# Performance work log

Measured on AMD Instinct MI355X. Metric: run time of the kernel, lower is better.

Reference implementation:

```python
import jax, jax.numpy as jnp
import numpy as np

B, N, DIM = 8, 2048, 1024
DR = DIM // 4      # MoE feature dim = 256
E, DH = 4, DIM // 32  # 4 experts, hidden 32
TASKS = 3
TOPK = 2


def _ln(x, g, b, eps=1e-5):
    m = x.mean(-1, keepdims=True)
    v = x.var(-1, keepdims=True)
    return (x - m) * jax.lax.rsqrt(v + eps) * g + b


def _cv_sq(x, eps=1e-10):
    # squared coefficient of variation (Shazeer MoE load-balance loss)
    return x.var() / (x.mean() ** 2 + eps)


def setup_inputs() -> dict:
    key = jax.random.key(0)
    ks = jax.random.split(key, 14)
    g = lambda k, shape, sc: jax.random.normal(k, shape, jnp.float32) * sc
    return {
        "x": jax.random.normal(ks[0], (B, N, DIM), jnp.float32),
        "t": jax.random.normal(ks[1], (B, N, DIM), jnp.float32),
        "past_x": jax.random.normal(ks[2], (B, N, DIM), jnp.float32),
        "past_t": jax.random.normal(ks[3], (B, N, DIM), jnp.float32),
        "task_index": 1,
        "ln1_g": jnp.ones((2 * DIM,), jnp.float32),
        "ln1_b": jnp.zeros((2 * DIM,), jnp.float32),
        "w_red": g(ks[4], (2 * DIM, DR), 0.03),       # xavier-ish, stored [in,out]
        "ln2_g": jnp.ones((DR,), jnp.float32),
        "ln2_b": jnp.zeros((DR,), jnp.float32),
        "w_gate": g(ks[5], (TASKS, DR, E), 0.02),      # per-task gating weights
        "w1": g(ks[6], (E, DR, DH), 0.05),
        "b1": jnp.zeros((E, DH), jnp.float32),
        "w2": g(ks[7], (E, DH, DR), 0.05),
        "b2": jnp.zeros((E, DR), jnp.float32),
        "modal_shifts": g(ks[8], (2 * TASKS, DIM), 0.02),
        "ws1": g(ks[9], (DIM, DIM), 0.02),             # score_net Linear(dim,dim)
        "ws2": g(ks[10], (DIM, 1), 0.02),              # score_net Linear(dim,1)
    }


def reference(x, t, past_x, past_t, task_index, ln1_g, ln1_b, w_red, ln2_g, ln2_b,
              w_gate, w1, b1, w2, b2, modal_shifts, ws1, ws2):
    Bx, Nx, C = x.shape
    y = jnp.concatenate([x, t], axis=-1)               # [B,N,2C]
    y = _ln(y, ln1_g, ln1_b)
    y = y @ w_red                                      # [B,N,C//4]
    y = _ln(y, ln2_g, ln2_b)
    yf = y.reshape(Bx * Nx, C // 4)                    # [M,256]

    # ---- MMoE: noisy top-k gating (eval: no noise), k=2 over E=4 experts ----
    logits = yf @ w_gate[task_index]                   # [M,E]
    top_v, top_i = jax.lax.top_k(logits, TOPK)         # [M,k]
    top_g = jax.nn.softmax(top_v, axis=-1)
    M = yf.shape[0]
    gates = jnp.zeros_like(logits).at[jnp.arange(M)[:, None], top_i].set(top_g)  # [M,E]
    h = jax.nn.relu(jnp.einsum('md,edh->meh', yf, w1) + b1)   # [M,E,32]
    eo = jnp.einsum('meh,eho->meo', h, w2) + b2               # [M,E,256]
    ymoe = jnp.einsum('meo,me->mo', eo, gates)                # [M,256]
    importance = gates.sum(0)
    load = (gates > 0).astype(jnp.float32).sum(0)
    aux_loss = _cv_sq(importance) + _cv_sq(load)

    ymoe = ymoe.reshape(Bx, Nx, C // 4)
    prompt_x, prompt_t = jnp.split(ymoe, 2, axis=-1)   # [B,N,C//8] each
    # AdaptiveAvgPool1d(1) over last dim + sigmoid -> [B,N,1] gate
    prompt_x = jax.nn.sigmoid(prompt_x.mean(-1, keepdims=True))
    prompt_t = jax.nn.sigmoid(prompt_t.mean(-1, keepdims=True))

    out_x = prompt_x * x + modal_shifts[task_index * 2 + 0]
    out_t = prompt_t * t + modal_shifts[task_index * 2 + 1]

    # delta / score-net softmax combine (past_xft branch)
    d1 = jnp.abs(out_x - past_x).mean(axis=1)          # [B,C]
    d2 = jnp.abs(out_t - past_t).mean(axis=1)
    s1 = jax.nn.relu(d1 @ ws1) @ ws2                   # [B,1]
    s2 = jax.nn.relu(d2 @ ws1) @ ws2
    w = jax.nn.softmax(jnp.concatenate([s1, s2], axis=1), axis=1)  # [B,2]
    out = w[:, 1, None, None] * out_x + w[:, 0, None, None] * out_t
    return out, aux_loss, out_x, out_t
```

## Files before the change

kernel.cpp:

```cpp
#include <hip/hip_runtime.h>
#include <math.h>

#define DIMC 1024
#define C2   2048
#define DR   256
#define DH   32
#define NE   4
#define NB   8
#define NN   2048
#define NM   16384

typedef short bf16x8 __attribute__((ext_vector_type(8)));
typedef float f32x4  __attribute__((ext_vector_type(4)));

__device__ __forceinline__ unsigned short f2bf(float f) {
    union { float f; unsigned int u; } v; v.f = f;
    unsigned int r = v.u + 0x7fffu + ((v.u >> 16) & 1u);
    return (unsigned short)(r >> 16);
}

__global__ __launch_bounds__(256) void k_prep(
    const float* __restrict__ wred, const float* __restrict__ g1,
    const float* __restrict__ b1v, unsigned short* __restrict__ wpp,
    float* __restrict__ u, float* __restrict__ beta)
{
    __shared__ unsigned short tsh[64][72];
    __shared__ float ush[64], bsh[64];
    const int tid = threadIdx.x;
    const int k0 = (blockIdx.x >> 2) * 64;
    const int c0 = (blockIdx.x & 3) * 64;
    if (tid < 64) { ush[tid] = 0.f; bsh[tid] = 0.f; }
    __syncthreads();

    const int r = tid >> 2, cs = (tid & 3) * 16;
    const float gk = g1[k0 + r], bk = b1v[k0 + r];
#pragma unroll
    for (int i = 0; i < 4; ++i) {
        float4 wv = *(const float4*)(wred + (size_t)(k0 + r) * DR + c0 + cs + i * 4);
        const int cb = cs + i * 4;
        atomicAdd(&ush[cb + 0], gk * wv.x); atomicAdd(&ush[cb + 1], gk * wv.y);
        atomicAdd(&ush[cb + 2], gk * wv.z); atomicAdd(&ush[cb + 3], gk * wv.w);
        atomicAdd(&bsh[cb + 0], bk * wv.x); atomicAdd(&bsh[cb + 1], bk * wv.y);
        atomicAdd(&bsh[cb + 2], bk * wv.z); atomicAdd(&bsh[cb + 3], bk * wv.w);
        tsh[cb + 0][r] = f2bf(gk * wv.x);
        tsh[cb + 1][r] = f2bf(gk * wv.y);
        tsh[cb + 2][r] = f2bf(gk * wv.z);
        tsh[cb + 3][r] = f2bf(gk * wv.w);
    }
    __syncthreads();

    const int cc = tid >> 2, seg = (tid & 3) * 16;
    uint4 v0 = *(const uint4*)&tsh[cc][seg];
    uint4 v1 = *(const uint4*)&tsh[cc][seg + 8];
    unsigned short* dst = wpp + (size_t)(c0 + cc) * C2 + k0 + seg;
    *(uint4*)(dst)     = v0;
    *(uint4*)(dst + 8) = v1;
    if (tid < 64) {
        atomicAdd(&u[c0 + tid],    ush[tid]);
        atomicAdd(&beta[c0 + tid], bsh[tid]);
    }
}

#define FT  64
#define FBK 64
#define LDA 72
#define LDB 72

__global__ __launch_bounds__(256) void k_front(
    const float* __restrict__ x, const float* __restrict__ t,
    const unsigned short* __restrict__ wpp,
    const float* __restrict__ u, const float* __restrict__ beta,
    const float* __restrict__ ln2g, const float* __restrict__ ln2b,
    float* __restrict__ yf)
{
    __shared__ unsigned short A_sh[FT * LDA];
    __shared__ unsigned short B_sh[DR * LDB];
    __shared__ float us_sh[DR], be_sh[DR], g2_sh[DR], b2_sh[DR];
    __shared__ float mean_sh[FT], rstd_sh[FT];
    __shared__ float pls[FT][2], plss[FT][2];

    const int tid  = threadIdx.x;
    const int m0   = blockIdx.x * FT;
    const int lane = tid & 63;
    const int w    = tid >> 6;
    const int wr   = w & 1, wc = w >> 1;
    const int cl   = lane & 15, kg = lane >> 4;

    if (tid < DR) {
        us_sh[tid] = u[tid];   be_sh[tid] = beta[tid];
        g2_sh[tid] = ln2g[tid]; b2_sh[tid] = ln2b[tid];
    }

    const int atok = tid >> 2, aks = (tid & 3) * 16;
    const int brow = tid >> 3, boff = (tid & 7) * 8;

    float s1 = 0.f, ss1 = 0.f;
    float4 ax[4];
    uint4  bw[8];

    {
        const float* arow = x + (size_t)(m0 + atok) * DIMC + aks;
#pragma unroll
        for (int i = 0; i < 4; ++i) ax[i] = *(const float4*)(arow + i * 4);
#pragma unroll
        for (int i = 0; i < 8; ++i)
            bw[i] = *(const uint4*)(wpp + (size_t)(i * 32 + brow) * C2 + boff);
    }

    f32x4 acc[2][8];
#pragma unroll
    for (int rt = 0; rt < 2; ++rt)
#pragma unroll
        for (int ct = 0; ct < 8; ++ct) acc[rt][ct] = (f32x4){0.f, 0.f, 0.f, 0.f};

    for (int kc = 0; kc < 32; ++kc) {
        __syncthreads();
#pragma unroll
        for (int i = 0; i < 4; ++i) {
            float4 v = ax[i];
            s1  += v.x + v.y + v.z + v.w;
            ss1 += v.x * v.x + v.y * v.y + v.z * v.z + v.w * v.w;
            short4 p;
            p.x = (short)f2bf(v.x); p.y = (short)f2bf(v.y);
            p.z = (short)f2bf(v.z); p.w = (short)f2bf(v.w);
            *(short4*)&A_sh[atok * LDA + aks + i * 4] = p;
        }
#pragma unroll
        for (int i = 0; i < 8; ++i)
            *(uint4*)&B_sh[(i * 32 + brow) * LDB + boff] = bw[i];
        __syncthreads();

        if (kc < 31) {
            const int kn = kc + 1;
            const float* src = (kn < 16) ? x : t;
            const int kb = (kn < 16) ? kn * FBK : (kn - 16) * FBK;
            const float* arow = src + (size_t)(m0 + atok) * DIMC + kb + aks;
#pragma unroll
            for (int i = 0; i < 4; ++i) ax[i] = *(const float4*)(arow + i * 4);
#pragma unroll
            for (int i = 0; i < 8; ++i)
                bw[i] = *(const uint4*)(wpp + (size_t)(i * 32 + brow) * C2 + kn * FBK + boff);
        }

#pragma unroll
        for (int kk = 0; kk < 2; ++kk) {
            bf16x8 af0 = *(const bf16x8*)&A_sh[(wr * 32 + 0  + cl) * LDA + kk * 32 + kg * 8];
            bf16x8 af1 = *(const bf16x8*)&A_sh[(wr * 32 + 16 + cl) * LDA + kk * 32 + kg * 8];
#pragma unroll
            for (int ct = 0; ct < 8; ++ct) {
                bf16x8 bf = *(const bf16x8*)&B_sh[(wc * 128 + ct * 16 + cl) * LDB + kk * 32 + kg * 8];
                acc[0][ct] = __builtin_amdgcn_mfma_f32_16x16x32_bf16(af0, bf, acc[0][ct], 0, 0, 0);
                acc[1][ct] = __builtin_amdgcn_mfma_f32_16x16x32_bf16(af1, bf, acc[1][ct], 0, 0, 0);
            }
        }
    }

    {
        float s = s1, ss = ss1;
        s += __shfl_xor(s, 1); ss += __shfl_xor(ss, 1);
        s += __shfl_xor(s, 2); ss += __shfl_xor(ss, 2);
        if ((tid & 3) == 0) {
            float m  = s * (1.f / 2048.f);
            float va = ss * (1.f / 2048.f) - m * m;
            mean_sh[atok] = m;
            rstd_sh[atok] = rsqrtf(va + 1e-5f);
        }
    }
    __syncthreads();

    float rsum[2][4], rssq[2][4];
#pragma unroll
    for (int rt = 0; rt < 2; ++rt)
#pragma unroll
        for (int reg = 0; reg < 4; ++reg) { rsum[rt][reg] = 0.f; rssq[rt][reg] = 0.f; }

#pragma unroll
    for (int rt = 0; rt < 2; ++rt) {
#pragma unroll
        for (int ct = 0; ct < 8; ++ct) {
            const int col = wc * 128 + ct * 16 + cl;
            const float uu = us_sh[col], bb = be_sh[col];
#pragma unroll
            for (int reg = 0; reg < 4; ++reg) {
                const int tok = wr * 32 + rt * 16 + kg * 4 + reg;
                const float mu = mean_sh[tok], rr = rstd_sh[tok];
                float y = rr * acc[rt][ct][reg] - rr * mu * uu + bb;
                acc[rt][ct][reg] = y;
                rsum[rt][reg] += y; rssq[rt][reg] += y * y;
            }
        }
    }
#pragma unroll
    for (int mask = 1; mask <= 8; mask <<= 1)
#pragma unroll
        for (int rt = 0; rt < 2; ++rt)
#pragma unroll
            for (int reg = 0; reg < 4; ++reg) {
                rsum[rt][reg] += __shfl_xor(rsum[rt][reg], mask);
                rssq[rt][reg] += __shfl_xor(rssq[rt][reg], mask);
            }
    if (cl == 0) {
#pragma unroll
        for (int rt = 0; rt < 2; ++rt)
#pragma unroll
            for (int reg = 0; reg < 4; ++reg) {
                const int tok = wr * 32 + rt * 16 + kg * 4 + reg;
                pls[tok][wc]  = rsum[rt][reg];
                plss[tok][wc] = rssq[rt][reg];
            }
    }
    __syncthreads();

#pragma unroll
    for (int rt = 0; rt < 2; ++rt) {
#pragma unroll
        for (int reg = 0; reg < 4; ++reg) {
            const int tok = wr * 32 + rt * 16 + kg * 4 + reg;
            const float m2 = (pls[tok][0] + pls[tok][1]) * (1.f / 256.f);
            const float v2 = (plss[tok][0] + plss[tok][1]) * (1.f / 256.f) - m2 * m2;
            const float r2 = rsqrtf(v2 + 1e-5f);
            float* yr = yf + (size_t)(m0 + tok) * DR;
#pragma unroll
            for (int ct = 0; ct < 8; ++ct) {
                const int col = wc * 128 + ct * 16 + cl;
                yr[col] = (acc[rt][ct][reg] - m2) * r2 * g2_sh[col] + b2_sh[col];
            }
        }
    }
}

__global__ __launch_bounds__(256) void k_moe(
    const float* __restrict__ yf, const int* __restrict__ taskp,
    const float* __restrict__ wgate,
    const float* __restrict__ w1, const float* __restrict__ b1,
    const float* __restrict__ w2, const float* __restrict__ b2,
    float* __restrict__ px, float* __restrict__ pt,
    double* __restrict__ imp, double* __restrict__ loadc)
{
    __shared__ float yf_sh[4][DR];
    __shared__ float hg_sh[4][2][DH];
    __shared__ float red_sh[8];

    const int tid = threadIdx.x, w = tid >> 6, l = tid & 63;
    if (tid < 8) red_sh[tid] = 0.f;
    const int task = *taskp;
    const int m = blockIdx.x * 4 + w;

    float4 v4 = *(const float4*)(yf + (size_t)m * DR + l * 4);
    *(float4*)&yf_sh[w][l * 4] = v4;
    __syncthreads();

    const float* wg = wgate + task * (DR * NE);
    float lg0 = 0.f, lg1 = 0.f, lg2 = 0.f, lg3 = 0.f;
    {
        const float vv[4] = {v4.x, v4.y, v4.z, v4.w};
#pragma unroll
        for (int i = 0; i < 4; ++i) {
            float4 wrow = *(const float4*)(wg + (l * 4 + i) * 4);
            float a = vv[i];
            lg0 += a * wrow.x; lg1 += a * wrow.y;
            lg2 += a * wrow.z; lg3 += a * wrow.w;
        }
    }
#pragma unroll
    for (int off = 32; off; off >>= 1) {
        lg0 += __shfl_xor(lg0, off); lg1 += __shfl_xor(lg1, off);
        lg2 += __shfl_xor(lg2, off); lg3 += __shfl_xor(lg3, off);
    }
    float lg[4] = {lg0, lg1, lg2, lg3};

    int i0 = 0; float v0 = lg[0];
#pragma unroll
    for (int e = 1; e < 4; ++e) if (lg[e] > v0) { v0 = lg[e]; i0 = e; }
    int i1 = -1; float v1 = -INFINITY;
#pragma unroll
    for (int e = 0; e < 4; ++e) if (e != i0 && lg[e] > v1) { v1 = lg[e]; i1 = e; }
    const float g1 = 1.f / (1.f + expf(v0 - v1));
    const float g0 = 1.f - g1;

    const int half = l >> 5, j = l & 31;
    const int e    = half ? i1 : i0;
    const float ge = half ? g1 : g0;
    const float* w1e = w1 + e * (DR * DH) + j;
    float h = b1[e * DH + j];
#pragma unroll 4
    for (int c = 0; c < DR; c += 4) {
        float4 y4 = *(const float4*)&yf_sh[w][c];
        h += y4.x * w1e[(c + 0) * DH] + y4.y * w1e[(c + 1) * DH]
           + y4.z * w1e[(c + 2) * DH] + y4.w * w1e[(c + 3) * DH];
    }
    hg_sh[w][half][j] = ge * fmaxf(h, 0.f);
    __syncthreads();

    const int o0 = l * 4;
    float4 ym;
    {
        float4 ba = *(const float4*)(b2 + i0 * DR + o0);
        float4 bb = *(const float4*)(b2 + i1 * DR + o0);
        ym.x = g0 * ba.x + g1 * bb.x;
        ym.y = g0 * ba.y + g1 * bb.y;
        ym.z = g0 * ba.z + g1 * bb.z;
        ym.w = g0 * ba.w + g1 * bb.w;
    }
    const float* w2a = w2 + i0 * (DH * DR) + o0;
    const float* w2b = w2 + i1 * (DH * DR) + o0;
#pragma unroll 4
    for (int jj = 0; jj < DH; ++jj) {
        float ha = hg_sh[w][0][jj], hb = hg_sh[w][1][jj];
        float4 wa = *(const float4*)(w2a + jj * DR);
        float4 wb = *(const float4*)(w2b + jj * DR);
        ym.x += ha * wa.x + hb * wb.x;
        ym.y += ha * wa.y + hb * wb.y;
        ym.z += ha * wa.z + hb * wb.z;
        ym.w += ha * wa.w + hb * wb.w;
    }

    float sm = ym.x + ym.y + ym.z + ym.w;
    float sx = (l < 32) ? sm : 0.f;
    float st = (l < 32) ? 0.f : sm;
#pragma unroll
    for (int off = 32; off; off >>= 1) { sx += __shfl_xor(sx, off); st += __shfl_xor(st, off); }
    if (l == 0) {
        px[m] = 1.f / (1.f + expf(-sx * (1.f / 128.f)));
        pt[m] = 1.f / (1.f + expf(-st * (1.f / 128.f)));
        atomicAdd(&red_sh[i0], g0);
        atomicAdd(&red_sh[i1], g1);
        atomicAdd(&red_sh[4 + i0], 1.f);
        atomicAdd(&red_sh[4 + i1], 1.f);
    }
    __syncthreads();
    if (tid < 4)        atomicAdd(&imp[tid], (double)red_sh[tid]);
    else if (tid < 8)   atomicAdd(&loadc[tid - 4], (double)red_sh[tid]);
}

#define K3T 32
__global__ __launch_bounds__(256) void k_outxt(
    const float* __restrict__ x, const float* __restrict__ t,
    const float* __restrict__ past_x, const float* __restrict__ past_t,
    const float* __restrict__ px, const float* __restrict__ pt,
    const int* __restrict__ taskp, const float* __restrict__ mshift,
    float* __restrict__ out_x, float* __restrict__ out_t,
    float* __restrict__ d1, float* __restrict__ d2)
{
    __shared__ float oxs[DIMC], ots[DIMC];
    const int b  = blockIdx.x >> 6;
    const int ch = blockIdx.x & 63;
    const int tid = threadIdx.x;
    const int c  = tid * 4;
    const int task = *taskp;

    float4 shx = *(const float4*)(mshift + (size_t)(task * 2 + 0) * DIMC + c);
    float4 sht = *(const float4*)(mshift + (size_t)(task * 2 + 1) * DIMC + c);

    float a10 = 0.f, a11 = 0.f, a12 = 0.f, a13 = 0.f;
    float a20 = 0.f, a21 = 0.f, a22 = 0.f, a23 = 0.f;
    const int mbase = b * NN + ch * K3T;

    for (int n = 0; n < K3T; ++n) {
        const int m = mbase + n;
        const size_t off = (size_t)m * DIMC + c;
        const float pxv = px[m], ptv = pt[m];

        float4 xv = *(const float4*)(x + off);
        float4 p1 = *(const float4*)(past_x + off);
        float4 ox;
        ox.x = pxv * xv.x + shx.x; ox.y = pxv * xv.y + shx.y;
        ox.z = pxv * xv.z + shx.z; ox.w = pxv * xv.w + shx.w;
        a10 += fabsf(ox.x - p1.x); a11 += fabsf(ox.y - p1.y);
        a12 += fabsf(ox.z - p1.z); a13 += fabsf(ox.w - p1.w);
        *(float4*)&oxs[c] = ox;

        float4 tv = *(const float4*)(t + off);
        float4 p2 = *(const float4*)(past_t + off);
        float4 ot;
        ot.x = ptv * tv.x + sht.x; ot.y = ptv * tv.y + sht.y;
        ot.z = ptv * tv.z + sht.z; ot.w = ptv * tv.w + sht.w;
        a20 += fabsf(ot.x - p2.x); a21 += fabsf(ot.y - p2.y);
        a22 += fabsf(ot.z - p2.z); a23 += fabsf(ot.w - p2.w);
        *(float4*)&ots[c] = ot;
        __syncthreads();

        const size_t rb = (size_t)m * DIMC;
        if (tid < 255) {
            const int cj = 3 + 4 * tid;
            float4 vx = make_float4(oxs[cj], oxs[cj+1], oxs[cj+2], oxs[cj+3]);
            *(float4*)(out_x + rb + cj) = vx;
            float4 vt = make_float4(ots[cj], ots[cj+1], ots[cj+2], ots[cj+3]);
            *(float4*)(out_t + rb + cj) = vt;
        } else {
            out_x[rb + 0] = oxs[0]; out_x[rb + 1] = oxs[1];
            out_x[rb + 2] = oxs[2]; out_x[rb + 1023] = oxs[1023];
            out_t[rb + 0] = ots[0]; out_t[rb + 1] = ots[1];
            out_t[rb + 2] = ots[2]; out_t[rb + 1023] = ots[1023];
        }
        __syncthreads();
    }
    atomicAdd(&d1[b * DIMC + c + 0], a10);
    atomicAdd(&d1[b * DIMC + c + 1], a11);
    atomicAdd(&d1[b * DIMC + c + 2], a12);
    atomicAdd(&d1[b * DIMC + c + 3], a13);
    atomicAdd(&d2[b * DIMC + c + 0], a20);
    atomicAdd(&d2[b * DIMC + c + 1], a21);
    atomicAdd(&d2[b * DIMC + c + 2], a22);
    atomicAdd(&d2[b * DIMC + c + 3], a23);
}

__global__ __launch_bounds__(256) void k_score(
    const float* __restrict__ d1, const float* __restrict__ d2,
    const float* __restrict__ ws1, const float* __restrict__ ws2,
    float* __restrict__ sv)
{
    __shared__ float red1[4][64], red2[4][64];
    const int tid = threadIdx.x;
    const int b = blockIdx.x >> 4, jc = blockIdx.x & 15;
    const int j = jc * 64 + (tid & 63), part = tid >> 6;
    const float* d1r = d1 + b * DIMC + part * 256;
    const float* d2r = d2 + b * DIMC + part * 256;
    const float* wp  = ws1 + (size_t)(part * 256) * DIMC + j;

    float acc1 = 0.f, acc2 = 0.f;
    for (int i = 0; i < 256; ++i) {
        float w = wp[(size_t)i * DIMC];
        acc1 += d1r[i] * w;
        acc2 += d2r[i] * w;
    }
    red1[part][tid & 63] = acc1;
    red2[part][tid & 63] = acc2;
    __syncthreads();
    if (tid < 64) {
        float h1 = red1[0][tid] + red1[1][tid] + red1[2][tid] + red1[3][tid];
        float h2 = red2[0][tid] + red2[1][tid] + red2[2][tid] + red2[3][tid];
        const int jj = jc * 64 + tid;
        float s1 = fmaxf(h1 * (1.f / NN), 0.f) * ws2[jj];
        float s2 = fmaxf(h2 * (1.f / NN), 0.f) * ws2[jj];
#pragma unroll
        for (int mask = 1; mask <= 32; mask <<= 1) {
            s1 += __shfl_xor(s1, mask); s2 += __shfl_xor(s2, mask);
        }
        if (tid == 0) {
            atomicAdd(&sv[b * 2 + 0], s1);
            atomicAdd(&sv[b * 2 + 1], s2);
        }
    }
}

__global__ void k_final_small(const double* __restrict__ imp, const double* __restrict__ loadc,
                              const float* __restrict__ sv, float* __restrict__ wcomb,
                              float* __restrict__ aux_out)
{
    const int tid = threadIdx.x;
    if (tid == 0) {
        double mi = 0, qi = 0, ml = 0, ql = 0;
        for (int e = 0; e < 4; ++e) {
            mi += imp[e]; qi += imp[e] * imp[e];
            ml += loadc[e]; ql += loadc[e] * loadc[e];
        }
        mi *= 0.25; qi *= 0.25; ml *= 0.25; ql *= 0.25;
        double vi = qi - mi * mi, vl = ql - ml * ml;
        *aux_out = (float)(vi / (mi * mi + 1e-10) + vl / (ml * ml + 1e-10));
    }
    if (tid < 8) {
        float s1 = sv[tid * 2 + 0], s2 = sv[tid * 2 + 1];
        float mx = fmaxf(s1, s2);
        float e1 = expf(s1 - mx), e2 = expf(s2 - mx);
        float inv = 1.f / (e1 + e2);
        wcomb[tid * 2 + 0] = e2 * inv;
        wcomb[tid * 2 + 1] = e1 * inv;
    }
}

__global__ __launch_bounds__(256) void k_combine(
    const float* __restrict__ out_x, const float* __restrict__ out_t,
    const float* __restrict__ wcomb, float* __restrict__ out)
{
    __shared__ float oxs[DIMC], ots[DIMC];
    const int m = blockIdx.x;
    const size_t rb = (size_t)m * DIMC;
    const int b = m >> 11;
    const float wx = wcomb[b * 2 + 0], wt = wcomb[b * 2 + 1];
    const int tid = threadIdx.x;

    if (tid < 255) {
        const int cj = 3 + 4 * tid;
        float4 vx = *(const float4*)(out_x + rb + cj);
        oxs[cj] = vx.x; oxs[cj + 1] = vx.y; oxs[cj + 2] = vx.z; oxs[cj + 3] = vx.w;
        float4 vt = *(const float4*)(out_t + rb + cj);
        ots[cj] = vt.x; ots[cj + 1] = vt.y; ots[cj + 2] = vt.z; ots[cj + 3] = vt.w;
    } else {
        oxs[0] = out_x[rb + 0]; oxs[1] = out_x[rb + 1];
        oxs[2] = out_x[rb + 2]; oxs[1023] = out_x[rb + 1023];
        ots[0] = out_t[rb + 0]; ots[1] = out_t[rb + 1];
        ots[2] = out_t[rb + 2]; ots[1023] = out_t[rb + 1023];
    }
    __syncthreads();

    const int c = tid * 4;
    float4 o;
    o.x = wx * oxs[c + 0] + wt * ots[c + 0];
    o.y = wx * oxs[c + 1] + wt * ots[c + 1];
    o.z = wx * oxs[c + 2] + wt * ots[c + 2];
    o.w = wx * oxs[c + 3] + wt * ots[c + 3];
    *(float4*)(out + rb + c) = o;
}

extern "C" void kernel_launch(void* const* d_in, const int* in_sizes, int n_in,
                              void* d_out, int out_size, void* d_ws, size_t ws_size,
                              hipStream_t stream)
{
    const float* x      = (const float*)d_in[0];
    const float* t      = (const float*)d_in[1];
    const float* past_x = (const float*)d_in[2];
    const float* past_t = (const float*)d_in[3];
    const int*   task   = (const int*)d_in[4];
    const float* ln1g   = (const float*)d_in[5];
    const float* ln1b   = (const float*)d_in[6];
    const float* wred   = (const float*)d_in[7];
    const float* ln2g   = (const float*)d_in[8];
    const float* ln2b   = (const float*)d_in[9];
    const float* wgate  = (const float*)d_in[10];
    const float* w1     = (const float*)d_in[11];
    const float* b1     = (const float*)d_in[12];
    const float* w2     = (const float*)d_in[13];
    const float* b2     = (const float*)d_in[14];
    const float* mshift = (const float*)d_in[15];
    const float* ws1    = (const float*)d_in[16];
    const float* ws2    = (const float*)d_in[17];

    float* f     = (float*)d_ws;
    float* d1    = f;
    float* d2    = f + 8192;
    float* sv    = f + 16384;
    float* wcomb = f + 16400;
    double* imp   = (double*)(f + 16416);
    double* loadc = (double*)(f + 16424);

    float* out   = (float*)d_out;
    float* aux   = out + (size_t)NM * DIMC;
    float* out_x = aux + 1;
    float* out_t = out_x + (size_t)NM * DIMC;

    float* yf  = out;
    unsigned short* wpp = (unsigned short*)(out + 8000000);
    float* u    = out + 8400000;
    float* beta = out + 8400256;
    float* px   = out + (size_t)NM * DIMC - 2 * NM;
    float* pt   = px + NM;

    hipMemsetAsync(d_ws, 0, 16432 * sizeof(float), stream);
    hipMemsetAsync(u, 0, 512 * sizeof(float), stream);

    k_prep<<<128, 256, 0, stream>>>(wred, ln1g, ln1b, wpp, u, beta);
    k_front<<<NM / FT, 256, 0, stream>>>(x, t, wpp, u, beta, ln2g, ln2b, yf);
    k_moe<<<NM / 4, 256, 0, stream>>>(yf, task, wgate, w1, b1, w2, b2, px, pt, imp, loadc);
    k_outxt<<<NB * (NN / K3T), 256, 0, stream>>>(x, t, past_x, past_t, px, pt, task,
                                                 mshift, out_x, out_t, d1, d2);
    k_score<<<128, 256, 0, stream>>>(d1, d2, ws1, ws2, sv);
    k_final_small<<<1, 64, 0, stream>>>(imp, loadc, sv, wcomb, aux);
    k_combine<<<NM, 256, 0, stream>>>(out_x, out_t, wcomb, out);
}
```

Baseline: 715.0 us.

## Double-buffer front GEMM with direct global-to-LDS weight loads and smaller tiles

Reworks the fused LayerNorm and reduction GEMM kernel. It uses 32-token tiles with four waves each covering 64 output columns, double-buffered LDS, and global_load_lds to stream the bf16 weight tile straight into XOR-swizzled shared memory. Activation loads and bf16 conversion for the next chunk overlap the MFMA work on the current one. The aim is more blocks in flight (launch bounds of two per CU), fewer register staging copies and fewer LDS bank conflicts. In exchange, weight tiles are reloaded twice as often per token, since each block covers fewer tokens.

```diff
diff --git a/kernel.cpp b/kernel.cpp
--- a/kernel.cpp
+++ b/kernel.cpp
@@ -61,29 +61,33 @@
     }
 }
 
-#define FT  64
-#define FBK 64
-#define LDA 72
-#define LDB 72
-
-__global__ __launch_bounds__(256) void k_front(
+#define FT   32
+#define FBK  64
+#define LDA  72
+#define NCH  32
+
+#define GLDS(gp, lo) __builtin_amdgcn_global_load_lds( \
+    (const __attribute__((address_space(1))) unsigned int*)(unsigned long long)(gp), \
+    (__attribute__((address_space(3))) unsigned int*)(unsigned int)(unsigned long long)(lo), \
+    16, 0, 0)
+
+__global__ __launch_bounds__(256, 2) void k_front(
     const float* __restrict__ x, const float* __restrict__ t,
     const unsigned short* __restrict__ wpp,
     const float* __restrict__ u, const float* __restrict__ beta,
     const float* __restrict__ ln2g, const float* __restrict__ ln2b,
     float* __restrict__ yf)
 {
-    __shared__ unsigned short A_sh[FT * LDA];
-    __shared__ unsigned short B_sh[DR * LDB];
+    __shared__ __attribute__((aligned(16))) unsigned short A_sh[2][FT * LDA];
+    __shared__ __attribute__((aligned(16))) unsigned short B_sh[2][DR * FBK];
     __shared__ float us_sh[DR], be_sh[DR], g2_sh[DR], b2_sh[DR];
     __shared__ float mean_sh[FT], rstd_sh[FT];
-    __shared__ float pls[FT][2], plss[FT][2];
+    __shared__ float pls[FT][4], plss[FT][4];
 
     const int tid  = threadIdx.x;
     const int m0   = blockIdx.x * FT;
     const int lane = tid & 63;
     const int w    = tid >> 6;
-    const int wr   = w & 1, wc = w >> 1;
     const int cl   = lane & 15, kg = lane >> 4;
 
     if (tid < DR) {
@@ -91,75 +95,92 @@
         g2_sh[tid] = ln2g[tid]; b2_sh[tid] = ln2b[tid];
     }
 
-    const int atok = tid >> 2, aks = (tid & 3) * 16;
-    const int brow = tid >> 3, boff = (tid & 7) * 8;
+    const int atok = tid >> 3;
+    const int aks  = (tid & 7) * 8;
+
+    const int brow  = w * 64 + (lane >> 3);
+    const int bslot = (lane & 7) ^ (lane >> 3);
+    const unsigned char* wppB =
+        (const unsigned char*)wpp + (size_t)brow * 4096 + (size_t)bslot * 16;
+    const unsigned long long ldsB =
+        (unsigned long long)(const void*)&B_sh[0][0] + (unsigned)(w * 8192);
 
     float s1 = 0.f, ss1 = 0.f;
-    float4 ax[4];
-    uint4  bw[8];
-
-    {
-        const float* arow = x + (size_t)(m0 + atok) * DIMC + aks;
-#pragma unroll
-        for (int i = 0; i < 4; ++i) ax[i] = *(const float4*)(arow + i * 4);
-#pragma unroll
-        for (int i = 0; i < 8; ++i)
-            bw[i] = *(const uint4*)(wpp + (size_t)(i * 32 + brow) * C2 + boff);
-    }
-
-    f32x4 acc[2][8];
+    f32x4 acc[2][4];
 #pragma unroll
     for (int rt = 0; rt < 2; ++rt)
 #pragma unroll
-        for (int ct = 0; ct < 8; ++ct) acc[rt][ct] = (f32x4){0.f, 0.f, 0.f, 0.f};
-
-    for (int kc = 0; kc < 32; ++kc) {
+        for (int ct = 0; ct < 4; ++ct) acc[rt][ct] = (f32x4){0.f, 0.f, 0.f, 0.f};
+
+    float4 nax0, nax1;
+
+#define STAGE(KN, BUF) do { \
+        const float* _src = ((KN) < 16) ? x : t; \
+        const float* _ar = _src + (size_t)(m0 + atok) * DIMC + ((KN) & 15) * FBK + aks; \
+        nax0 = *(const float4*)_ar; nax1 = *(const float4*)(_ar + 4); \
+        _Pragma("unroll") \
+        for (int _i = 0; _i < 8; ++_i) \
+            GLDS(wppB + (size_t)_i * 8 * 4096 + (KN) * 128, \
+                 ldsB + (unsigned)((BUF) * 32768 + _i * 1024)); \
+    } while (0)
+
+#define CVT(BUF) do { \
+        float4 _v = nax0; \
+        s1 += _v.x + _v.y + _v.z + _v.w; \
+        ss1 += _v.x*_v.x + _v.y*_v.y + _v.z*_v.z + _v.w*_v.w; \
+        short4 _p; \
+        _p.x = (short)f2bf(_v.x); _p.y = (short)f2bf(_v.y); \
+        _p.z = (short)f2bf(_v.z); _p.w = (short)f2bf(_v.w); \
+        *(short4*)&A_sh[BUF][atok * LDA + aks] = _p; \
+        _v = nax1; \
+        s1 += _v.x + _v.y + _v.z + _v.w; \
+        ss1 += _v.x*_v.x + _v.y*_v.y + _v.z*_v.z + _v.w*_v.w; \
+        _p.x = (short)f2bf(_v.x); _p.y = (short)f2bf(_v.y); \
+        _p.z = (short)f2bf(_v.z); _p.w = (short)f2bf(_v.w); \
+        *(short4*)&A_sh[BUF][atok * LDA + aks + 4] = _p; \
+    } while (0)
+
+#define MFMA_PHASE(BUF) do { \
+        _Pragma("unroll") \
+        for (int kk = 0; kk < 2; ++kk) { \
+            bf16x8 af0 = *(const bf16x8*)&A_sh[BUF][(cl)      * LDA + kk * 32 + kg * 8]; \
+            bf16x8 af1 = *(const bf16x8*)&A_sh[BUF][(16 + cl) * LDA + kk * 32 + kg * 8]; \
+            _Pragma("unroll") \
+            for (int ct = 0; ct < 4; ++ct) { \
+                const int _r  = w * 64 + ct * 16 + cl; \
+                const int _off = (_r * 128 + kk * 64 + kg * 16) ^ ((_r & 7) << 4); \
+                bf16x8 bf = *(const bf16x8*)((const char*)&B_sh[BUF][0] + _off); \
+                acc[0][ct] = __builtin_amdgcn_mfma_f32_16x16x32_bf16(af0, bf, acc[0][ct], 0, 0, 0); \
+                acc[1][ct] = __builtin_amdgcn_mfma_f32_16x16x32_bf16(af1, bf, acc[1][ct], 0, 0, 0); \
+            } \
+        } \
+    } while (0)
+
+    STAGE(0, 0);
+    CVT(0);
+    __syncthreads();
+
+    for (int kc = 0; kc < NCH; kc += 2) {
+        STAGE(kc + 1, 1);
+        MFMA_PHASE(0);
+        CVT(1);
         __syncthreads();
-#pragma unroll
-        for (int i = 0; i < 4; ++i) {
-            float4 v = ax[i];
-            s1  += v.x + v.y + v.z + v.w;
-            ss1 += v.x * v.x + v.y * v.y + v.z * v.z + v.w * v.w;
-            short4 p;
-            p.x = (short)f2bf(v.x); p.y = (short)f2bf(v.y);
-            p.z = (short)f2bf(v.z); p.w = (short)f2bf(v.w);
-            *(short4*)&A_sh[atok * LDA + aks + i * 4] = p;
-        }
-#pragma unroll
-        for (int i = 0; i < 8; ++i)
-            *(uint4*)&B_sh[(i * 32 + brow) * LDB + boff] = bw[i];
+        if (kc + 2 < NCH) {
+            STAGE(kc + 2, 0);
+            MFMA_PHASE(1);
+            CVT(0);
+        } else {
+            MFMA_PHASE(1);
+        }
         __syncthreads();
-
-        if (kc < 31) {
-            const int kn = kc + 1;
-            const float* src = (kn < 16) ? x : t;
-            const int kb = (kn < 16) ? kn * FBK : (kn - 16) * FBK;
-            const float* arow = src + (size_t)(m0 + atok) * DIMC + kb + aks;
-#pragma unroll
-            for (int i = 0; i < 4; ++i) ax[i] = *(const float4*)(arow + i * 4);
-#pragma unroll
-            for (int i = 0; i < 8; ++i)
-                bw[i] = *(const uint4*)(wpp + (size_t)(i * 32 + brow) * C2 + kn * FBK + boff);
-        }
-
-#pragma unroll
-        for (int kk = 0; kk < 2; ++kk) {
-            bf16x8 af0 = *(const bf16x8*)&A_sh[(wr * 32 + 0  + cl) * LDA + kk * 32 + kg * 8];
-            bf16x8 af1 = *(const bf16x8*)&A_sh[(wr * 32 + 16 + cl) * LDA + kk * 32 + kg * 8];
-#pragma unroll
-            for (int ct = 0; ct < 8; ++ct) {
-                bf16x8 bf = *(const bf16x8*)&B_sh[(wc * 128 + ct * 16 + cl) * LDB + kk * 32 + kg * 8];
-                acc[0][ct] = __builtin_amdgcn_mfma_f32_16x16x32_bf16(af0, bf, acc[0][ct], 0, 0, 0);
-                acc[1][ct] = __builtin_amdgcn_mfma_f32_16x16x32_bf16(af1, bf, acc[1][ct], 0, 0, 0);
-            }
-        }
     }
 
     {
         float s = s1, ss = ss1;
         s += __shfl_xor(s, 1); ss += __shfl_xor(ss, 1);
         s += __shfl_xor(s, 2); ss += __shfl_xor(ss, 2);
-        if ((tid & 3) == 0) {
+        s += __shfl_xor(s, 4); ss += __shfl_xor(ss, 4);
+        if ((tid & 7) == 0) {
             float m  = s * (1.f / 2048.f);
             float va = ss * (1.f / 2048.f) - m * m;
             mean_sh[atok] = m;
@@ -175,20 +196,19 @@
         for (int reg = 0; reg < 4; ++reg) { rsum[rt][reg] = 0.f; rssq[rt][reg] = 0.f; }
 
 #pragma unroll
-    for (int rt = 0; rt < 2; ++rt) {
-#pragma unroll
-        for (int ct = 0; ct < 8; ++ct) {
-            const int col = wc * 128 + ct * 16 + cl;
-            const float uu = us_sh[col], bb = be_sh[col];
+    for (int ct = 0; ct < 4; ++ct) {
+        const int col = w * 64 + ct * 16 + cl;
+        const float uu = us_sh[col], bb = be_sh[col];
+#pragma unroll
+        for (int rt = 0; rt < 2; ++rt)
 #pragma unroll
             for (int reg = 0; reg < 4; ++reg) {
-                const int tok = wr * 32 + rt * 16 + kg * 4 + reg;
+                const int tok = rt * 16 + kg * 4 + reg;
                 const float mu = mean_sh[tok], rr = rstd_sh[tok];
                 float y = rr * acc[rt][ct][reg] - rr * mu * uu + bb;
                 acc[rt][ct][reg] = y;
                 rsum[rt][reg] += y; rssq[rt][reg] += y * y;
             }
-        }
     }
 #pragma unroll
     for (int mask = 1; mask <= 8; mask <<= 1)
@@ -204,9 +224,9 @@
         for (int rt = 0; rt < 2; ++rt)
 #pragma unroll
             for (int reg = 0; reg < 4; ++reg) {
-                const int tok = wr * 32 + rt * 16 + kg * 4 + reg;
-                pls[tok][wc]  = rsum[rt][reg];
-                plss[tok][wc] = rssq[rt][reg];
+                const int tok = rt * 16 + kg * 4 + reg;
+                pls[tok][w]  = rsum[rt][reg];
+                plss[tok][w] = rssq[rt][reg];
             }
     }
     __syncthreads();
@@ -215,18 +235,21 @@
     for (int rt = 0; rt < 2; ++rt) {
 #pragma unroll
         for (int reg = 0; reg < 4; ++reg) {
-            const int tok = wr * 32 + rt * 16 + kg * 4 + reg;
-            const float m2 = (pls[tok][0] + pls[tok][1]) * (1.f / 256.f);
-            const float v2 = (plss[tok][0] + plss[tok][1]) * (1.f / 256.f) - m2 * m2;
+            const int tok = rt * 16 + kg * 4 + reg;
+            const float m2 = (pls[tok][0] + pls[tok][1] + pls[tok][2] + pls[tok][3]) * (1.f / 256.f);
+            const float v2 = (plss[tok][0] + plss[tok][1] + plss[tok][2] + plss[tok][3]) * (1.f / 256.f) - m2 * m2;
             const float r2 = rsqrtf(v2 + 1e-5f);
             float* yr = yf + (size_t)(m0 + tok) * DR;
 #pragma unroll
-            for (int ct = 0; ct < 8; ++ct) {
-                const int col = wc * 128 + ct * 16 + cl;
+            for (int ct = 0; ct < 4; ++ct) {
+                const int col = w * 64 + ct * 16 + cl;
                 yr[col] = (acc[rt][ct][reg] - m2) * r2 * g2_sh[col] + b2_sh[col];
             }
         }
     }
+#undef STAGE
+#undef CVT
+#undef MFMA_PHASE
 }
 
 __global__ __launch_bounds__(256) void k_moe(
```

Result: faster. 602.7 us (-15.7%).
